# Optimization experiments

Measured on AMD Instinct MI355X. Metric: run time of the kernel, lower is better.

The kernel has to match this reference:

```python
import jax, jax.numpy as jnp
import numpy as np

ALPHA = 0.5
NOISE_KEY = jax.random.key(42)  # fixed key: deterministic stand-in for torch.randn


def setup_inputs() -> dict:
    key = jax.random.key(0)
    k1, k2 = jax.random.split(key)
    N, D, E = 8192, 1024, 131072
    x = jax.random.normal(k1, (N, D), dtype=jnp.float32)
    edge_index = jax.random.randint(k2, (2, E), 0, N, dtype=jnp.int64)
    return {"x": x, "edge_index": edge_index}


def reference(x, edge_index):
    # edge_index is accepted but unused, matching the original module.
    N = x.shape[0]
    m = jax.random.normal(NOISE_KEY, (N, N), dtype=x.dtype)  # [N, N] noise
    M = jax.nn.softmax(m / ALPHA, axis=1)                    # row-wise Gibbs weights
    return M @ x                                             # [N, D]
```

## Files before the change

### kernel.cpp

```cpp
#include <hip/hip_runtime.h>
#include <stdint.h>
#include <stddef.h>

#define NROWS 8192
#define NCOLS 8192
#define DDIM  1024

typedef float  f32x4 __attribute__((ext_vector_type(4)));
typedef _Float16 f16x8 __attribute__((ext_vector_type(8)));

#if __has_builtin(__builtin_amdgcn_exp2f)
#define EXP2F(x) __builtin_amdgcn_exp2f(x)
#else
#define EXP2F(x) exp2f(x)
#endif
#if __has_builtin(__builtin_amdgcn_logf)
#define LOG2F(x) __builtin_amdgcn_logf(x)
#else
#define LOG2F(x) log2f(x)
#endif
#if __has_builtin(__builtin_amdgcn_sqrtf)
#define SQRTF(x) __builtin_amdgcn_sqrtf(x)
#else
#define SQRTF(x) sqrtf(x)
#endif

__device__ __forceinline__ uint32_t rotl32(uint32_t x, uint32_t r){
  return (x << r) | (x >> (32u - r));
}

__device__ __forceinline__ void threefry2x32(uint32_t x0, uint32_t x1,
                                             uint32_t& o0, uint32_t& o1){
  const uint32_t k0 = 0u, k1 = 42u;
  const uint32_t k2 = k0 ^ k1 ^ 0x1BD11BDAu;
  x0 += k0; x1 += k1;
#define TF_R(r) { x0 += x1; x1 = rotl32(x1, r); x1 ^= x0; }
  TF_R(13) TF_R(15) TF_R(26) TF_R(6)
  x0 += k1; x1 += k2 + 1u;
  TF_R(17) TF_R(29) TF_R(16) TF_R(24)
  x0 += k2; x1 += k0 + 2u;
  TF_R(13) TF_R(15) TF_R(26) TF_R(6)
  x0 += k0; x1 += k1 + 3u;
  TF_R(17) TF_R(29) TF_R(16) TF_R(24)
  x0 += k1; x1 += k2 + 4u;
  TF_R(13) TF_R(15) TF_R(26) TF_R(6)
  x0 += k2; x1 += k0 + 5u;
#undef TF_R
  o0 = x0; o1 = x1;
}

__device__ __forceinline__ float elemE(uint32_t f){
  uint32_t o0, o1;
  threefry2x32(0u, f, o0, o1);
  const uint32_t b = o0 ^ o1;
  float u = __uint_as_float((b >> 9) | 0x3F800000u) - 1.0f;
  const float lo = -0.99999994f;
  float v = fmaf(u, 2.0f, lo);
  v = fmaxf(v, lo);
  const float t1 = fmaf(-v, v, 1.0f);
  float w = LOG2F(t1) * (-0.69314718f);
  float p;
  if (w < 5.0f){
    w -= 2.5f;
    p =              3.97426473e-08f;
    p = fmaf(p, w,   4.85465e-07f);
    p = fmaf(p, w,  -4.98283e-06f);
    p = fmaf(p, w,  -6.21053e-06f);
    p = fmaf(p, w,   3.09120e-04f);
    p = fmaf(p, w,  -1.77290e-03f);
    p = fmaf(p, w,  -5.90817e-03f);
    p = fmaf(p, w,   3.48803163e-01f);
    p = fmaf(p, w,   2.12331355e+00f);
  } else {
    w = SQRTF(w) - 3.0f;
    p =             -2.83147363e-04f;
    p = fmaf(p, w,   1.42765560e-04f);
    p = fmaf(p, w,   1.90825981e-03f);
    p = fmaf(p, w,  -5.19500608e-03f);
    p = fmaf(p, w,   8.11688602e-03f);
    p = fmaf(p, w,  -1.07798386e-02f);
    p = fmaf(p, w,   1.33487061e-02f);
    p = fmaf(p, w,   1.41658096e+00f);
    p = fmaf(p, w,   4.00643396e+00f);
  }
  const float m = p * v;
  return EXP2F(fmaf(m, 2.8853900817779268f, -4.0f));
}

__device__ __forceinline__ uint16_t f2h(float a){
  union { _Float16 h; uint16_t u; } c; c.h = (_Float16)a; return c.u;
}

__global__ __launch_bounds__(256) void transpose_cast(const float* __restrict__ x,
                                                      uint16_t* __restrict__ xT){
  __shared__ float tile[32][33];
  const int tx = threadIdx.x & 31;
  const int ty = threadIdx.x >> 5;
  const int dcol = blockIdx.x * 32;
  const int nrow = blockIdx.y * 32;
  #pragma unroll
  for (int r = 0; r < 32; r += 8)
    tile[ty + r][tx] = x[(size_t)(nrow + ty + r) * DDIM + dcol + tx];
  __syncthreads();
  #pragma unroll
  for (int r = 0; r < 32; r += 8)
    xT[(size_t)(dcol + ty + r) * NROWS + nrow + tx] = f2h(tile[tx][ty + r]);
}

__global__ __launch_bounds__(256) void gen_trans_rows(const float* __restrict__ x,
                                                      uint16_t* __restrict__ xT,
                                                      uint16_t* __restrict__ P,
                                                      float* __restrict__ S){
  const int t = threadIdx.x;
  {
    __shared__ float tile[32][33];
    const int tx = t & 31;
    const int ty = t >> 5;
    const int dcol = (blockIdx.x & 31) * 32;
    const int nrow = (blockIdx.x >> 5) * 32;
    #pragma unroll
    for (int r = 0; r < 32; r += 8)
      tile[ty + r][tx] = x[(size_t)(nrow + ty + r) * DDIM + dcol + tx];
    __syncthreads();
    #pragma unroll
    for (int r = 0; r < 32; r += 8)
      xT[(size_t)(dcol + ty + r) * NROWS + nrow + tx] = f2h(tile[tx][ty + r]);
  }
  const int gi = blockIdx.x;
  const uint32_t base = (uint32_t)gi * 8192u;
  uint16_t* __restrict__ prow = P + (size_t)gi * NCOLS;
  float acc = 0.0f;
  #pragma unroll
  for (int g = 0; g < 4; ++g){
    const uint32_t j0 = (uint32_t)(g * 2048) + ((uint32_t)t << 3);
    float e[8];
    #pragma unroll
    for (int i = 0; i < 8; ++i){ e[i] = elemE(base + j0 + (uint32_t)i); acc += e[i]; }
    f16x8 pk;
    #pragma unroll
    for (int i = 0; i < 8; ++i) pk[i] = (_Float16)e[i];
    *reinterpret_cast<f16x8*>(prow + j0) = pk;
  }
  #pragma unroll
  for (int off = 32; off > 0; off >>= 1) acc += __shfl_down(acc, off, 64);
  __shared__ float sm[4];
  __syncthreads();
  if ((t & 63) == 0) sm[t >> 6] = acc;
  __syncthreads();
  if (t == 0) S[gi] = (sm[0] + sm[1]) + (sm[2] + sm[3]);
}

__global__ __launch_bounds__(256) void gen_rows(uint16_t* __restrict__ P,
                                                float* __restrict__ S, int row0){
  const int gi = row0 + blockIdx.x;
  const uint32_t base = (uint32_t)gi * 8192u;
  const int t = threadIdx.x;
  uint16_t* __restrict__ prow = P + (size_t)blockIdx.x * NCOLS;
  float acc = 0.0f;
  #pragma unroll
  for (int g = 0; g < 4; ++g){
    const uint32_t j0 = (uint32_t)(g * 2048) + ((uint32_t)t << 3);
    float e[8];
    #pragma unroll
    for (int i = 0; i < 8; ++i){ e[i] = elemE(base + j0 + (uint32_t)i); acc += e[i]; }
    f16x8 pk;
    #pragma unroll
    for (int i = 0; i < 8; ++i) pk[i] = (_Float16)e[i];
    *reinterpret_cast<f16x8*>(prow + j0) = pk;
  }
  #pragma unroll
  for (int off = 32; off > 0; off >>= 1) acc += __shfl_down(acc, off, 64);
  __shared__ float sm[4];
  if ((t & 63) == 0) sm[t >> 6] = acc;
  __syncthreads();
  if (t == 0) S[gi] = (sm[0] + sm[1]) + (sm[2] + sm[3]);
}

typedef const __attribute__((address_space(1))) void GAS;
typedef __attribute__((address_space(3))) void LAS;

__device__ __forceinline__ void gload16(const void* g, void* l){
  __builtin_amdgcn_global_load_lds((GAS*)g, (LAS*)l, 16, 0, 0);
}

#define BM 128
#define BN 128
#define BK 64

__global__ __launch_bounds__(256, 3) void gemm_rows(
    const uint16_t* __restrict__ P,
    const uint16_t* __restrict__ xT,
    const float* __restrict__ S,
    int row0,
    float* __restrict__ O)
{
  __shared__ uint16_t smem[16384];
  uint16_t* As = smem;
  uint16_t* Bs = smem + 8192;

  const int tid  = threadIdx.x;
  const int lane = tid & 63;
  const int wave = tid >> 6;
  const int wr = (wave >> 1) * 64;
  const int wc = (wave & 1) * 64;
  const int l15 = lane & 15;
  const int lq  = lane >> 4;

  const size_t m0 = (size_t)blockIdx.x * BM;
  const size_t n0 = (size_t)blockIdx.y * BN;

  const int srow = tid >> 3;
  const int sx   = (tid & 7) ^ (srow & 7);
  const uint16_t* gA = P  + (m0 + srow) * (size_t)NCOLS + sx * 8;
  const uint16_t* gB = xT + (n0 + srow) * (size_t)NCOLS + sx * 8;

  f32x4 acc[4][4];
  #pragma unroll
  for (int i = 0; i < 4; ++i)
    #pragma unroll
    for (int j = 0; j < 4; ++j)
      #pragma unroll
      for (int q = 0; q < 4; ++q) acc[i][j][q] = 0.0f;

  const int axor = l15 & 7;

  for (int k0 = 0; k0 < NCOLS; k0 += BK){
    #pragma unroll
    for (int r = 0; r < 4; ++r)
      gload16(gA + (size_t)(32 * r) * NCOLS + k0, As + (tid + 256 * r) * 8);
    #pragma unroll
    for (int r = 0; r < 4; ++r)
      gload16(gB + (size_t)(32 * r) * NCOLS + k0, Bs + (tid + 256 * r) * 8);
    __syncthreads();
    #pragma unroll
    for (int ks = 0; ks < 2; ++ks){
      const int kphys = ((lq + 4 * ks) ^ axor) * 8;
      f16x8 af[4], bfrag[4];
      #pragma unroll
      for (int i = 0; i < 4; ++i)
        af[i] = *reinterpret_cast<const f16x8*>(As + (wr + i*16 + l15) * BK + kphys);
      #pragma unroll
      for (int j = 0; j < 4; ++j)
        bfrag[j] = *reinterpret_cast<const f16x8*>(Bs + (wc + j*16 + l15) * BK + kphys);
      #pragma unroll
      for (int i = 0; i < 4; ++i)
        #pragma unroll
        for (int j = 0; j < 4; ++j)
          acc[i][j] = __builtin_amdgcn_mfma_f32_16x16x32_f16(af[i], bfrag[j], acc[i][j], 0, 0, 0);
    }
    __syncthreads();
  }

  #pragma unroll
  for (int i = 0; i < 4; ++i){
    float rinv[4];
    #pragma unroll
    for (int r = 0; r < 4; ++r)
      rinv[r] = 1.0f / S[row0 + m0 + wr + i*16 + lq*4 + r];
    #pragma unroll
    for (int j = 0; j < 4; ++j){
      const size_t col = n0 + wc + j*16 + l15;
      #pragma unroll
      for (int r = 0; r < 4; ++r){
        const size_t row = m0 + wr + i*16 + lq*4 + r;
        O[row * DDIM + col] = acc[i][j][r] * rinv[r];
      }
    }
  }
}

#define GM 256
#define GN 128
#define GK 64
#define GNT (NCOLS / GK)
#define GBUF 24576

__global__ __launch_bounds__(512, 2) void gemm256(
    const uint16_t* __restrict__ P,
    const uint16_t* __restrict__ xT,
    const float* __restrict__ S,
    float* __restrict__ O)
{
  extern __shared__ uint16_t sm[];

  const int tid  = threadIdx.x;
  const int lane = tid & 63;
  const int wave = tid >> 6;
  const int wr = (wave >> 1) * 64;
  const int wc = (wave & 1) * 64;
  const int l15 = lane & 15;
  const int lq  = lane >> 4;
  const int axor = l15 & 7;

  const int b   = blockIdx.x;
  const int swz = (b & 7) * 32 + (b >> 3);
  const size_t m0 = (size_t)(swz & 31) * GM;
  const size_t n0 = (size_t)(swz >> 5) * GN;

  const int srow = tid >> 3;
  const int sx   = (tid & 7) ^ (srow & 7);
  const uint16_t* gA = P  + (m0 + srow) * (size_t)NCOLS + sx * 8;
  const uint16_t* gB = xT + (n0 + srow) * (size_t)NCOLS + sx * 8;

  uint16_t* buf0 = sm;
  uint16_t* buf1 = sm + GBUF;
  uint16_t* buf2 = sm + 2 * GBUF;

  auto STAGE = [&](uint16_t* base, int kt){
    const int kk = kt * GK;
    #pragma unroll
    for (int r = 0; r < 4; ++r)
      gload16(gA + (size_t)(64 * r) * NCOLS + kk, base + (tid + 512 * r) * 8);
    #pragma unroll
    for (int r = 0; r < 2; ++r)
      gload16(gB + (size_t)(64 * r) * NCOLS + kk, base + 16384 + (tid + 512 * r) * 8);
  };

  f32x4 acc[4][4];
  #pragma unroll
  for (int i = 0; i < 4; ++i)
    #pragma unroll
    for (int j = 0; j < 4; ++j)
      #pragma unroll
      for (int q = 0; q < 4; ++q) acc[i][j][q] = 0.0f;

  STAGE(buf0, 0);
  STAGE(buf1, 1);
  asm volatile("s_waitcnt vmcnt(6)" ::: "memory");
  __builtin_amdgcn_s_barrier();

  uint16_t *pc = buf0, *pn = buf1, *ps = buf2;
  for (int t = 0; t < GNT; ++t){
    if (t + 2 < GNT) STAGE(ps, t + 2);

    f16x8 af[2][4], bf[2][4];
    #pragma unroll
    for (int ks = 0; ks < 2; ++ks){
      const int kphys = ((lq + 4 * ks) ^ axor) * 8;
      #pragma unroll
      for (int i = 0; i < 4; ++i)
        af[ks][i] = *reinterpret_cast<const f16x8*>(pc + (wr + i*16 + l15) * GK + kphys);
      #pragma unroll
      for (int j = 0; j < 4; ++j)
        bf[ks][j] = *reinterpret_cast<const f16x8*>(pc + 16384 + (wc + j*16 + l15) * GK + kphys);
    }

    __builtin_amdgcn_s_setprio(1);
    #pragma unroll
    for (int ks = 0; ks < 2; ++ks)
      #pragma unroll
      for (int i = 0; i < 4; ++i)
        #pragma unroll
        for (int j = 0; j < 4; ++j)
          acc[i][j] = __builtin_amdgcn_mfma_f32_16x16x32_f16(af[ks][i], bf[ks][j], acc[i][j], 0, 0, 0);
    __builtin_amdgcn_s_setprio(0);

    if (t + 2 < GNT) asm volatile("s_waitcnt vmcnt(6) lgkmcnt(0)" ::: "memory");
    else             asm volatile("s_waitcnt vmcnt(0) lgkmcnt(0)" ::: "memory");
    __builtin_amdgcn_s_barrier();

    uint16_t* tmp = pc; pc = pn; pn = ps; ps = tmp;
  }

  #pragma unroll
  for (int i = 0; i < 4; ++i){
    float rinv[4];
    #pragma unroll
    for (int r = 0; r < 4; ++r)
      rinv[r] = 1.0f / S[m0 + wr + i*16 + lq*4 + r];
    #pragma unroll
    for (int j = 0; j < 4; ++j){
      const size_t col = n0 + wc + j*16 + l15;
      #pragma unroll
      for (int r = 0; r < 4; ++r){
        const size_t row = m0 + wr + i*16 + lq*4 + r;
        O[row * DDIM + col] = acc[i][j][r] * rinv[r];
      }
    }
  }
}

extern "C" void kernel_launch(void* const* d_in, const int* in_sizes, int n_in,
                              void* d_out, int out_size, void* d_ws, size_t ws_size,
                              hipStream_t stream)
{
  (void)in_sizes; (void)n_in; (void)out_size;
  const float* x = (const float*)d_in[0];
  float* O = (float*)d_out;
  uint8_t* ws = (uint8_t*)d_ws;

  float* S = (float*)ws;
  const size_t S_bytes = (size_t)NROWS * sizeof(float);
  uint16_t* xT = (uint16_t*)(ws + S_bytes);
  const size_t xT_bytes = (size_t)DDIM * NROWS * sizeof(uint16_t);
  uint16_t* P = (uint16_t*)(ws + S_bytes + xT_bytes);
  const size_t used = S_bytes + xT_bytes;
  const size_t avail = ws_size > used ? ws_size - used : 0;

  const size_t fullP = (size_t)NROWS * NCOLS * sizeof(uint16_t);
  if (avail >= fullP){
    gen_trans_rows<<<NROWS, 256, 0, stream>>>(x, xT, P, S);
    gemm256<<<dim3(256), 512, 3 * GBUF * sizeof(uint16_t), stream>>>(P, xT, S, O);
  } else {
    transpose_cast<<<dim3(DDIM/32, NROWS/32), 256, 0, stream>>>(x, xT);
    int R = 128;
    for (int r = 4096; r >= 128; r >>= 1)
      if ((size_t)r * NCOLS * sizeof(uint16_t) <= avail){ R = r; break; }
    for (int r0 = 0; r0 < NROWS; r0 += R){
      gen_rows<<<R, 256, 0, stream>>>(P, S, r0);
      gemm_rows<<<dim3(R/BM, DDIM/BN), 256, 0, stream>>>(P, xT, S, r0, O + (size_t)r0 * DDIM);
    }
  }
}
```

Before: 353.2 us.

## Fuse softmax-noise generation into persistent GEMM with grid-wide phased sync

```diff
diff --git a/kernel.cpp b/kernel.cpp
--- a/kernel.cpp
+++ b/kernel.cpp
@@ -107,49 +107,6 @@
     xT[(size_t)(dcol + ty + r) * NROWS + nrow + tx] = f2h(tile[tx][ty + r]);
 }
 
-__global__ __launch_bounds__(256) void gen_trans_rows(const float* __restrict__ x,
-                                                      uint16_t* __restrict__ xT,
-                                                      uint16_t* __restrict__ P,
-                                                      float* __restrict__ S){
-  const int t = threadIdx.x;
-  {
-    __shared__ float tile[32][33];
-    const int tx = t & 31;
-    const int ty = t >> 5;
-    const int dcol = (blockIdx.x & 31) * 32;
-    const int nrow = (blockIdx.x >> 5) * 32;
-    #pragma unroll
-    for (int r = 0; r < 32; r += 8)
-      tile[ty + r][tx] = x[(size_t)(nrow + ty + r) * DDIM + dcol + tx];
-    __syncthreads();
-    #pragma unroll
-    for (int r = 0; r < 32; r += 8)
-      xT[(size_t)(dcol + ty + r) * NROWS + nrow + tx] = f2h(tile[tx][ty + r]);
-  }
-  const int gi = blockIdx.x;
-  const uint32_t base = (uint32_t)gi * 8192u;
-  uint16_t* __restrict__ prow = P + (size_t)gi * NCOLS;
-  float acc = 0.0f;
-  #pragma unroll
-  for (int g = 0; g < 4; ++g){
-    const uint32_t j0 = (uint32_t)(g * 2048) + ((uint32_t)t << 3);
-    float e[8];
-    #pragma unroll
-    for (int i = 0; i < 8; ++i){ e[i] = elemE(base + j0 + (uint32_t)i); acc += e[i]; }
-    f16x8 pk;
-    #pragma unroll
-    for (int i = 0; i < 8; ++i) pk[i] = (_Float16)e[i];
-    *reinterpret_cast<f16x8*>(prow + j0) = pk;
-  }
-  #pragma unroll
-  for (int off = 32; off > 0; off >>= 1) acc += __shfl_down(acc, off, 64);
-  __shared__ float sm[4];
-  __syncthreads();
-  if ((t & 63) == 0) sm[t >> 6] = acc;
-  __syncthreads();
-  if (t == 0) S[gi] = (sm[0] + sm[1]) + (sm[2] + sm[3]);
-}
-
 __global__ __launch_bounds__(256) void gen_rows(uint16_t* __restrict__ P,
                                                 float* __restrict__ S, int row0){
   const int gi = row0 + blockIdx.x;
@@ -188,11 +145,8 @@
 #define BK 64
 
 __global__ __launch_bounds__(256, 3) void gemm_rows(
-    const uint16_t* __restrict__ P,
-    const uint16_t* __restrict__ xT,
-    const float* __restrict__ S,
-    int row0,
-    float* __restrict__ O)
+    const uint16_t* __restrict__ P, const uint16_t* __restrict__ xT,
+    const float* __restrict__ S, int row0, float* __restrict__ O)
 {
   __shared__ uint16_t smem[16384];
   uint16_t* As = smem;
@@ -269,21 +223,28 @@
   }
 }
 
-#define GM 256
-#define GN 128
-#define GK 64
-#define GNT (NCOLS / GK)
-#define GBUF 24576
-
-__global__ __launch_bounds__(512, 2) void gemm256(
-    const uint16_t* __restrict__ P,
+#define PM 256
+#define PN 128
+#define PK 64
+#define TPC 16
+#define NCH 8
+#define PGBUF 24576
+
+__global__ __launch_bounds__(512, 2) void phased(
+    uint16_t* __restrict__ P,
     const uint16_t* __restrict__ xT,
-    const float* __restrict__ S,
+    float* S,
+    uint32_t* ctr,
     float* __restrict__ O)
 {
   extern __shared__ uint16_t sm[];
-
-  const int tid  = threadIdx.x;
+  const int tid = threadIdx.x;
+  const int b   = blockIdx.x;
+
+  const int swz = (b & 7) * 32 + (b >> 3);
+  const size_t m0 = (size_t)(swz & 31) * PM;
+  const size_t n0 = (size_t)(swz >> 5) * PN;
+
   const int lane = tid & 63;
   const int wave = tid >> 6;
   const int wr = (wave >> 1) * 64;
@@ -292,22 +253,35 @@
   const int lq  = lane >> 4;
   const int axor = l15 & 7;
 
-  const int b   = blockIdx.x;
-  const int swz = (b & 7) * 32 + (b >> 3);
-  const size_t m0 = (size_t)(swz & 31) * GM;
-  const size_t n0 = (size_t)(swz >> 5) * GN;
-
   const int srow = tid >> 3;
   const int sx   = (tid & 7) ^ (srow & 7);
   const uint16_t* gA = P  + (m0 + srow) * (size_t)NCOLS + sx * 8;
   const uint16_t* gB = xT + (n0 + srow) * (size_t)NCOLS + sx * 8;
 
   uint16_t* buf0 = sm;
-  uint16_t* buf1 = sm + GBUF;
-  uint16_t* buf2 = sm + 2 * GBUF;
+  uint16_t* buf1 = sm + PGBUF;
+  uint16_t* buf2 = sm + 2 * PGBUF;
+
+  const int grow = tid >> 4;
+  const int gl   = tid & 15;
+  const uint32_t growg = (uint32_t)(b * 32 + grow);
+  uint16_t* prow = P + (size_t)growg * NCOLS + gl * 4;
+  const uint32_t fbase = growg * 8192u + (uint32_t)(gl * 4);
+  float myS = 0.0f;
+
+  auto GEN4 = [&](int chunk, int kt){
+    const uint32_t f0 = fbase + (uint32_t)(chunk * 1024 + kt * 64);
+    float e0 = elemE(f0), e1 = elemE(f0 + 1u), e2 = elemE(f0 + 2u), e3 = elemE(f0 + 3u);
+    myS += (e0 + e1) + (e2 + e3);
+    union { _Float16 h[4]; uint64_t u; } pk;
+    pk.h[0] = (_Float16)e0; pk.h[1] = (_Float16)e1;
+    pk.h[2] = (_Float16)e2; pk.h[3] = (_Float16)e3;
+    __hip_atomic_store(reinterpret_cast<uint64_t*>(prow + chunk * 1024 + kt * 64),
+                       pk.u, __ATOMIC_RELAXED, __HIP_MEMORY_SCOPE_AGENT);
+  };
 
   auto STAGE = [&](uint16_t* base, int kt){
-    const int kk = kt * GK;
+    const int kk = kt * PK;
     #pragma unroll
     for (int r = 0; r < 4; ++r)
       gload16(gA + (size_t)(64 * r) * NCOLS + kk, base + (tid + 512 * r) * 8);
@@ -316,6 +290,20 @@
       gload16(gB + (size_t)(64 * r) * NCOLS + kk, base + 16384 + (tid + 512 * r) * 8);
   };
 
+  auto phase_sync = [&](uint32_t target){
+    asm volatile("s_waitcnt vmcnt(0) lgkmcnt(0)" ::: "memory");
+    __builtin_amdgcn_s_barrier();
+    if (tid == 0){
+      __hip_atomic_fetch_add(ctr, 1u, __ATOMIC_RELAXED, __HIP_MEMORY_SCOPE_AGENT);
+      int guard = 0;
+      while (__hip_atomic_load(ctr, __ATOMIC_RELAXED, __HIP_MEMORY_SCOPE_AGENT) < target){
+        __builtin_amdgcn_s_sleep(2);
+        if (++guard > (1 << 22)) break;
+      }
+    }
+    __builtin_amdgcn_s_barrier();
+  };
+
   f32x4 acc[4][4];
   #pragma unroll
   for (int i = 0; i < 4; ++i)
@@ -324,57 +312,80 @@
       #pragma unroll
       for (int q = 0; q < 4; ++q) acc[i][j][q] = 0.0f;
 
-  STAGE(buf0, 0);
-  STAGE(buf1, 1);
-  asm volatile("s_waitcnt vmcnt(6)" ::: "memory");
-  __builtin_amdgcn_s_barrier();
-
-  uint16_t *pc = buf0, *pn = buf1, *ps = buf2;
-  for (int t = 0; t < GNT; ++t){
-    if (t + 2 < GNT) STAGE(ps, t + 2);
-
-    f16x8 af[2][4], bf[2][4];
-    #pragma unroll
-    for (int ks = 0; ks < 2; ++ks){
-      const int kphys = ((lq + 4 * ks) ^ axor) * 8;
-      #pragma unroll
-      for (int i = 0; i < 4; ++i)
-        af[ks][i] = *reinterpret_cast<const f16x8*>(pc + (wr + i*16 + l15) * GK + kphys);
-      #pragma unroll
-      for (int j = 0; j < 4; ++j)
-        bf[ks][j] = *reinterpret_cast<const f16x8*>(pc + 16384 + (wc + j*16 + l15) * GK + kphys);
-    }
-
-    __builtin_amdgcn_s_setprio(1);
-    #pragma unroll
-    for (int ks = 0; ks < 2; ++ks)
-      #pragma unroll
-      for (int i = 0; i < 4; ++i)
+  for (int kt = 0; kt < TPC; ++kt) GEN4(0, kt);
+  phase_sync(256);
+
+  for (int c = 0; c < NCH; ++c){
+    const int kb = c * TPC;
+    const bool gen = (c + 1 < NCH);
+
+    STAGE(buf0, kb);
+    STAGE(buf1, kb + 1);
+    asm volatile("s_waitcnt vmcnt(6)" ::: "memory");
+    __builtin_amdgcn_s_barrier();
+
+    uint16_t *pc = buf0, *pn = buf1, *ps = buf2;
+    for (int t2 = 0; t2 < TPC; ++t2){
+      if (t2 + 2 < TPC) STAGE(ps, kb + t2 + 2);
+      if (gen) GEN4(c + 1, t2);
+
+      #pragma unroll
+      for (int ks = 0; ks < 2; ++ks){
+        const int kphys = ((lq + 4 * ks) ^ axor) * 8;
+        f16x8 af[4], bfrag[4];
+        #pragma unroll
+        for (int i = 0; i < 4; ++i)
+          af[i] = *reinterpret_cast<const f16x8*>(pc + (wr + i*16 + l15) * PK + kphys);
         #pragma unroll
         for (int j = 0; j < 4; ++j)
-          acc[i][j] = __builtin_amdgcn_mfma_f32_16x16x32_f16(af[ks][i], bf[ks][j], acc[i][j], 0, 0, 0);
-    __builtin_amdgcn_s_setprio(0);
-
-    if (t + 2 < GNT) asm volatile("s_waitcnt vmcnt(6) lgkmcnt(0)" ::: "memory");
-    else             asm volatile("s_waitcnt vmcnt(0) lgkmcnt(0)" ::: "memory");
-    __builtin_amdgcn_s_barrier();
-
-    uint16_t* tmp = pc; pc = pn; pn = ps; ps = tmp;
+          bfrag[j] = *reinterpret_cast<const f16x8*>(pc + 16384 + (wc + j*16 + l15) * PK + kphys);
+        __builtin_amdgcn_s_setprio(1);
+        #pragma unroll
+        for (int i = 0; i < 4; ++i)
+          #pragma unroll
+          for (int j = 0; j < 4; ++j)
+            acc[i][j] = __builtin_amdgcn_mfma_f32_16x16x32_f16(af[i], bfrag[j], acc[i][j], 0, 0, 0);
+        __builtin_amdgcn_s_setprio(0);
+      }
+
+      if (t2 + 2 < TPC){
+        if (gen) asm volatile("s_waitcnt vmcnt(7) lgkmcnt(0)" ::: "memory");
+        else     asm volatile("s_waitcnt vmcnt(6) lgkmcnt(0)" ::: "memory");
+      } else {
+        asm volatile("s_waitcnt vmcnt(0) lgkmcnt(0)" ::: "memory");
+      }
+      __builtin_amdgcn_s_barrier();
+      uint16_t* tmp = pc; pc = pn; pn = ps; ps = tmp;
+    }
+
+    if (c == NCH - 2){
+      float v = myS;
+      v += __shfl_down(v, 8, 16);
+      v += __shfl_down(v, 4, 16);
+      v += __shfl_down(v, 2, 16);
+      v += __shfl_down(v, 1, 16);
+      if (gl == 0)
+        __hip_atomic_store(&S[growg], v, __ATOMIC_RELAXED, __HIP_MEMORY_SCOPE_AGENT);
+    }
+    if (c + 1 < NCH) phase_sync(256u * (uint32_t)(c + 2));
   }
 
   #pragma unroll
   for (int i = 0; i < 4; ++i){
     float rinv[4];
     #pragma unroll
-    for (int r = 0; r < 4; ++r)
-      rinv[r] = 1.0f / S[m0 + wr + i*16 + lq*4 + r];
+    for (int r = 0; r < 4; ++r){
+      const float sv = __hip_atomic_load(&S[m0 + wr + i*16 + lq*4 + r],
+                                         __ATOMIC_RELAXED, __HIP_MEMORY_SCOPE_AGENT);
+      rinv[r] = 1.0f / sv;
+    }
     #pragma unroll
     for (int j = 0; j < 4; ++j){
       const size_t col = n0 + wc + j*16 + l15;
       #pragma unroll
       for (int r = 0; r < 4; ++r){
         const size_t row = m0 + wr + i*16 + lq*4 + r;
-        O[row * DDIM + col] = acc[i][j][r] * rinv[r];
+        __builtin_nontemporal_store(acc[i][j][r] * rinv[r], &O[row * DDIM + col]);
       }
     }
   }
@@ -390,17 +401,18 @@
   uint8_t* ws = (uint8_t*)d_ws;
 
   float* S = (float*)ws;
-  const size_t S_bytes = (size_t)NROWS * sizeof(float);
-  uint16_t* xT = (uint16_t*)(ws + S_bytes);
+  uint32_t* ctr = (uint32_t*)(ws + 32768);
+  uint16_t* xT = (uint16_t*)(ws + 32768 + 4096);
   const size_t xT_bytes = (size_t)DDIM * NROWS * sizeof(uint16_t);
-  uint16_t* P = (uint16_t*)(ws + S_bytes + xT_bytes);
-  const size_t used = S_bytes + xT_bytes;
+  uint16_t* P = (uint16_t*)(ws + 32768 + 4096 + xT_bytes);
+  const size_t used = 32768 + 4096 + xT_bytes;
   const size_t avail = ws_size > used ? ws_size - used : 0;
 
   const size_t fullP = (size_t)NROWS * NCOLS * sizeof(uint16_t);
   if (avail >= fullP){
-    gen_trans_rows<<<NROWS, 256, 0, stream>>>(x, xT, P, S);
-    gemm256<<<dim3(256), 512, 3 * GBUF * sizeof(uint16_t), stream>>>(P, xT, S, O);
+    hipMemsetAsync(ctr, 0, 4096, stream);
+    transpose_cast<<<dim3(DDIM/32, NROWS/32), 256, 0, stream>>>(x, xT);
+    phased<<<256, 512, 3 * PGBUF * sizeof(uint16_t), stream>>>(P, xT, S, ctr, O);
   } else {
     transpose_cast<<<dim3(DDIM/32, NROWS/32), 256, 0, stream>>>(x, xT);
     int R = 128;
```

Result: slower. 463.0 us (+31.1%).

## Interleave global prefetch with MFMA phases in 8-phase GEMM main loop

Applied to the files above, without the earlier changes.

```diff
diff --git a/kernel.cpp b/kernel.cpp
--- a/kernel.cpp
+++ b/kernel.cpp
@@ -188,11 +188,8 @@
 #define BK 64
 
 __global__ __launch_bounds__(256, 3) void gemm_rows(
-    const uint16_t* __restrict__ P,
-    const uint16_t* __restrict__ xT,
-    const float* __restrict__ S,
-    int row0,
-    float* __restrict__ O)
+    const uint16_t* __restrict__ P, const uint16_t* __restrict__ xT,
+    const float* __restrict__ S, int row0, float* __restrict__ O)
 {
   __shared__ uint16_t smem[16384];
   uint16_t* As = smem;
@@ -275,7 +272,7 @@
 #define GNT (NCOLS / GK)
 #define GBUF 24576
 
-__global__ __launch_bounds__(512, 2) void gemm256(
+__global__ __launch_bounds__(512, 2) void gemm8p(
     const uint16_t* __restrict__ P,
     const uint16_t* __restrict__ xT,
     const float* __restrict__ S,
@@ -306,15 +303,21 @@
   uint16_t* buf1 = sm + GBUF;
   uint16_t* buf2 = sm + 2 * GBUF;
 
-  auto STAGE = [&](uint16_t* base, int kt){
+  auto STAGE_A01 = [&](uint16_t* base, int kt){
     const int kk = kt * GK;
-    #pragma unroll
-    for (int r = 0; r < 4; ++r)
-      gload16(gA + (size_t)(64 * r) * NCOLS + kk, base + (tid + 512 * r) * 8);
-    #pragma unroll
-    for (int r = 0; r < 2; ++r)
-      gload16(gB + (size_t)(64 * r) * NCOLS + kk, base + 16384 + (tid + 512 * r) * 8);
+    gload16(gA + kk,                        base + tid * 8);
+    gload16(gA + (size_t)64 * NCOLS + kk,   base + (tid + 512) * 8);
   };
+  auto STAGE_A23 = [&](uint16_t* base, int kt){
+    const int kk = kt * GK;
+    gload16(gA + (size_t)128 * NCOLS + kk,  base + (tid + 1024) * 8);
+    gload16(gA + (size_t)192 * NCOLS + kk,  base + (tid + 1536) * 8);
+  };
+  auto STAGE_B = [&](uint16_t* base, int kt){
+    const int kk = kt * GK;
+    gload16(gB + kk,                        base + 16384 + tid * 8);
+    gload16(gB + (size_t)64 * NCOLS + kk,   base + 16384 + (tid + 512) * 8);
+  };
 
   f32x4 acc[4][4];
   #pragma unroll
@@ -324,41 +327,48 @@
       #pragma unroll
       for (int q = 0; q < 4; ++q) acc[i][j][q] = 0.0f;
 
-  STAGE(buf0, 0);
-  STAGE(buf1, 1);
-  asm volatile("s_waitcnt vmcnt(6)" ::: "memory");
-  __builtin_amdgcn_s_barrier();
+  STAGE_A01(buf0, 0); STAGE_A23(buf0, 0); STAGE_B(buf0, 0);
+  STAGE_A01(buf1, 1); STAGE_A23(buf1, 1); STAGE_B(buf1, 1);
 
   uint16_t *pc = buf0, *pn = buf1, *ps = buf2;
   for (int t = 0; t < GNT; ++t){
-    if (t + 2 < GNT) STAGE(ps, t + 2);
-
-    f16x8 af[2][4], bf[2][4];
+    if (t + 1 < GNT) asm volatile("s_waitcnt vmcnt(6)" ::: "memory");
+    else             asm volatile("s_waitcnt vmcnt(0)" ::: "memory");
+    __builtin_amdgcn_s_barrier();
+
+    const bool pre = (t + 2 < GNT);
+    f16x8 bf[2][4];
+
     #pragma unroll
     for (int ks = 0; ks < 2; ++ks){
-      const int kphys = ((lq + 4 * ks) ^ axor) * 8;
-      #pragma unroll
-      for (int i = 0; i < 4; ++i)
-        af[ks][i] = *reinterpret_cast<const f16x8*>(pc + (wr + i*16 + l15) * GK + kphys);
-      #pragma unroll
-      for (int j = 0; j < 4; ++j)
-        bf[ks][j] = *reinterpret_cast<const f16x8*>(pc + 16384 + (wc + j*16 + l15) * GK + kphys);
-    }
-
-    __builtin_amdgcn_s_setprio(1);
-    #pragma unroll
-    for (int ks = 0; ks < 2; ++ks)
-      #pragma unroll
-      for (int i = 0; i < 4; ++i)
+      #pragma unroll
+      for (int h = 0; h < 2; ++h){
+        const int kphys = ((lq + 4 * ks) ^ axor) * 8;
+        f16x8 af0 = *reinterpret_cast<const f16x8*>(pc + (wr + (2*h    )*16 + l15) * GK + kphys);
+        f16x8 af1 = *reinterpret_cast<const f16x8*>(pc + (wr + (2*h + 1)*16 + l15) * GK + kphys);
+        if (h == 0){
+          #pragma unroll
+          for (int j = 0; j < 4; ++j)
+            bf[ks][j] = *reinterpret_cast<const f16x8*>(pc + 16384 + (wc + j*16 + l15) * GK + kphys);
+        }
+        if (pre){
+          if      (ks == 0 && h == 0) STAGE_A01(ps, t + 2);
+          else if (ks == 0 && h == 1) STAGE_A23(ps, t + 2);
+          else if (ks == 1 && h == 0) STAGE_B  (ps, t + 2);
+        }
+        __builtin_amdgcn_s_barrier();
+        asm volatile("s_waitcnt lgkmcnt(0)" ::: "memory");
+        __builtin_amdgcn_s_setprio(1);
         #pragma unroll
         for (int j = 0; j < 4; ++j)
-          acc[i][j] = __builtin_amdgcn_mfma_f32_16x16x32_f16(af[ks][i], bf[ks][j], acc[i][j], 0, 0, 0);
-    __builtin_amdgcn_s_setprio(0);
-
-    if (t + 2 < GNT) asm volatile("s_waitcnt vmcnt(6) lgkmcnt(0)" ::: "memory");
-    else             asm volatile("s_waitcnt vmcnt(0) lgkmcnt(0)" ::: "memory");
-    __builtin_amdgcn_s_barrier();
-
+          acc[2*h    ][j] = __builtin_amdgcn_mfma_f32_16x16x32_f16(af0, bf[ks][j], acc[2*h    ][j], 0, 0, 0);
+        #pragma unroll
+        for (int j = 0; j < 4; ++j)
+          acc[2*h + 1][j] = __builtin_amdgcn_mfma_f32_16x16x32_f16(af1, bf[ks][j], acc[2*h + 1][j], 0, 0, 0);
+        __builtin_amdgcn_s_setprio(0);
+        __builtin_amdgcn_s_barrier();
+      }
+    }
     uint16_t* tmp = pc; pc = pn; pn = ps; ps = tmp;
   }
 
@@ -400,7 +410,7 @@
   const size_t fullP = (size_t)NROWS * NCOLS * sizeof(uint16_t);
   if (avail >= fullP){
     gen_trans_rows<<<NROWS, 256, 0, stream>>>(x, xT, P, S);
-    gemm256<<<dim3(256), 512, 3 * GBUF * sizeof(uint16_t), stream>>>(P, xT, S, O);
+    gemm8p<<<256, 512, 3 * GBUF * sizeof(uint16_t), stream>>>(P, xT, S, O);
   } else {
     transpose_cast<<<dim3(DDIM/32, NROWS/32), 256, 0, stream>>>(x, xT);
     int R = 128;
```

Result: no change. 356.9 us (+1.0%).
